# Kernel tuning notes

Measured on AMD Instinct MI355X. Metric: run time of the kernel, lower is better.

Reference implementation:

```python
import jax, jax.numpy as jnp
import numpy as np

H = 768  # bert-base hidden size; match MLP width = 2*H = 1536


def setup_inputs() -> dict:
    key = jax.random.key(0)
    ks = jax.random.split(key, 6)
    B, S = 2, 256
    std = 0.02  # TruncatedNormal(stddev=initializer_range)
    return {
        "hidden": jax.random.normal(ks[0], (B, S, H), dtype=jnp.float32),
        "w_start": jax.random.normal(ks[1], (H, 1), dtype=jnp.float32) * std,
        "b_start": jnp.zeros((1,), jnp.float32),
        "w_end": jax.random.normal(ks[2], (H, 1), dtype=jnp.float32) * std,
        "b_end": jnp.zeros((1,), jnp.float32),
        "w1": jax.random.normal(ks[3], (2 * H, 2 * H), dtype=jnp.float32) * std,
        "b1": jnp.zeros((2 * H,), jnp.float32),
        "w2": jax.random.normal(ks[4], (2 * H, 1), dtype=jnp.float32) * std,
        "b2": jnp.zeros((1,), jnp.float32),
    }


def reference(hidden, w_start, b_start, w_end, b_end, w1, b1, w2, b2):
    # hidden: [B, S, H] = BERT sequence output (dropout disabled at inference)
    start_logits = hidden @ w_start + b_start  # [B, S, 1]
    end_logits = hidden @ w_end + b_end        # [B, S, 1]

    # Pairwise span features: concat(row_i, col_j) along last dim, fed to dense1.
    # concat([row, col]) @ w1 == row @ w1[:H] + col @ w1[H:], so we split w1 and
    # broadcast-add instead of materializing the [B,S,S,2H] concat tile.
    row_proj = hidden @ w1[:H]   # [B, S, 2H] (start-token contribution)
    col_proj = hidden @ w1[H:]   # [B, S, 2H] (end-token contribution)
    pre = row_proj[:, :, None, :] + col_proj[:, None, :, :] + b1  # [B, S, S, 2H]
    act = jax.nn.gelu(pre, approximate=False)  # keras 'gelu' is exact
    match_logits = act @ w2 + b2  # [B, S, S, 1]
    return start_logits, end_logits, match_logits
```

## Files before the change

### kernel.cpp

```cpp
#include <hip/hip_runtime.h>
#include <stdint.h>

typedef __attribute__((ext_vector_type(8))) __bf16 bf16x8;
typedef __attribute__((ext_vector_type(4))) float  floatx4;
typedef __attribute__((ext_vector_type(4))) unsigned int uint4v;
typedef __attribute__((ext_vector_type(2))) unsigned int uint2v;
typedef __attribute__((ext_vector_type(4))) float  float4v;
typedef __attribute__((ext_vector_type(2))) _Float16 half2v;
typedef unsigned int u32;

__device__ __forceinline__ unsigned short f2bf(float f) {
  union { float f; unsigned int u; } x; x.f = f;
  unsigned int r = x.u + 0x7fffu + ((x.u >> 16) & 1u);
  return (unsigned short)(r >> 16);
}

__device__ __forceinline__ void gll16(const unsigned short* g, unsigned short* l) {
  __builtin_amdgcn_global_load_lds(
      (const __attribute__((address_space(1))) unsigned int*)g,
      (__attribute__((address_space(3))) unsigned int*)l, 16, 0, 0);
}

__global__ __launch_bounds__(256) void convert_kernel(
    const float* __restrict__ w1, unsigned short* __restrict__ Wfmt) {
  const int n  = blockIdx.x * 256 + threadIdx.x;
  const int qg = blockIdx.y;
  const float* src = w1 + (size_t)(qg * 8) * 1536 + n;
  uint4v o;
#pragma unroll
  for (int a = 0; a < 4; ++a) {
    u32 lo = f2bf(src[(size_t)(2 * a) * 1536]);
    u32 hi = f2bf(src[(size_t)(2 * a + 1) * 1536]);
    o[a] = lo | (hi << 16);
  }
  *(uint4v*)(Wfmt + ((size_t)qg * 1536 + n) * 8) = o;
}

__global__ __launch_bounds__(256) void proj_kernel(
    const float* __restrict__ hidden, const unsigned short* __restrict__ Wfmt,
    const float* __restrict__ b1, unsigned short* __restrict__ wsR,
    unsigned short* __restrict__ wsC,
    const float* __restrict__ w_start, const float* __restrict__ b_start,
    const float* __restrict__ w_end, const float* __restrict__ b_end,
    const float* __restrict__ b2, float* __restrict__ out) {
  const int tid  = threadIdx.x;
  if (blockIdx.y == 16) {
    if (blockIdx.x >= 32) {
      float v = b2[0];
      float4v vv = {v, v, v, v};
      int base = (blockIdx.x - 32) * 8192 + tid * 4;
#pragma unroll
      for (int itr = 0; itr < 8; ++itr)
        *(float4v*)(out + 1024 + base + itr * 1024) = vv;
      return;
    }
    const int lane = tid & 63;
    const int wv   = tid >> 6;
    const int wg   = blockIdx.x * 4 + wv;
    float wsv[12], wev[12];
#pragma unroll
    for (int t = 0; t < 12; ++t) {
      wsv[t] = w_start[lane + 64 * t];
      wev[t] = w_end[lane + 64 * t];
    }
    const float bs = b_start[0];
    const float be = b_end[0];
#pragma unroll
    for (int r = 0; r < 4; ++r) {
      int row = wg * 4 + r;
      const float* h = hidden + (size_t)row * 768;
      float ps = 0.f, pe = 0.f;
#pragma unroll
      for (int t = 0; t < 12; ++t) {
        float hv = h[lane + 64 * t];
        ps += hv * wsv[t];
        pe += hv * wev[t];
      }
#pragma unroll
      for (int off = 32; off >= 1; off >>= 1) {
        ps += __shfl_xor(ps, off, 64);
        pe += __shfl_xor(pe, off, 64);
      }
      if (lane == 0) { out[row] = ps + bs; out[512 + row] = pe + be; }
    }
    return;
  }

  __shared__ unsigned short As2[2][8 * 32 * 8];
  __shared__ unsigned short Bs2[2][8 * 64 * 8];

  const int lane = tid & 63;
  const int wave = tid >> 6;
  const int wr = wave >> 1, wc = wave & 1;
  const int m0 = blockIdx.y * 32;
  const int n0g = blockIdx.x * 64;
  const bool isR = (n0g < 1536);
  const int qgb = isR ? 0 : 96;
  const int n0 = isR ? n0g : (n0g - 1536);
  const int q4 = lane >> 4, l15 = lane & 15;

  floatx4 acc0 = {}, acc1 = {};

  const int a_row = tid >> 3;
  const int a_s   = tid & 7;
  const int aqh   = a_s >> 1;
  const int aj    = (a_s & 1) * 4;
  const float* hrow = hidden + (size_t)(m0 + a_row) * 768 + a_s * 4;

  const unsigned short* gB0 = Wfmt + ((size_t)(qgb + 2 * wave) * 1536 + n0 + lane) * 8;
  const unsigned short* gB1 = Wfmt + ((size_t)(qgb + 2 * wave + 1) * 1536 + n0 + lane) * 8;
  const size_t bstep = (size_t)8 * 1536 * 8;
  unsigned short* lB0 = &Bs2[0][(2 * wave) * 512];
  unsigned short* lB1 = &Bs2[0][(2 * wave + 1) * 512];
  unsigned short* lB0b = &Bs2[1][(2 * wave) * 512];
  unsigned short* lB1b = &Bs2[1][(2 * wave + 1) * 512];

#define PACKA(BUF, H, V)                                                     \
  {                                                                          \
    uint2v au_;                                                              \
    au_[0] = (u32)f2bf((V)[0]) | ((u32)f2bf((V)[1]) << 16);                  \
    au_[1] = (u32)f2bf((V)[2]) | ((u32)f2bf((V)[3]) << 16);                  \
    *(uint2v*)(&As2[BUF][(((H) * 4 + aqh) * 32 + a_row) * 8 + aj]) = au_;    \
  }

#define COMPUTE(BUF)                                                         \
  {                                                                          \
    _Pragma("unroll")                                                        \
    for (int ko2 = 0; ko2 < 2; ++ko2) {                                      \
      int qf = ko2 * 4 + q4;                                                 \
      bf16x8 af  = *(const bf16x8*)(&As2[BUF][(qf * 32 + 16 * wr + l15) * 8]); \
      bf16x8 bg0 = *(const bf16x8*)(&Bs2[BUF][(qf * 64 + 32 * wc + l15) * 8]); \
      bf16x8 bg1 = *(const bf16x8*)(&Bs2[BUF][(qf * 64 + 32 * wc + 16 + l15) * 8]); \
      acc0 = __builtin_amdgcn_mfma_f32_16x16x32_bf16(af, bg0, acc0, 0, 0, 0); \
      acc1 = __builtin_amdgcn_mfma_f32_16x16x32_bf16(af, bg1, acc1, 0, 0, 0); \
    }                                                                        \
  }

  gll16(gB0, lB0);
  gll16(gB1, lB1);
  float4v sA0 = *(const float4v*)(hrow);
  float4v sA1 = *(const float4v*)(hrow + 32);
  PACKA(0, 0, sA0); PACKA(0, 1, sA1);
  float4v sB0 = *(const float4v*)(hrow + 64);
  float4v sB1 = *(const float4v*)(hrow + 96);
  __syncthreads();

#pragma unroll
  for (int kb = 0; kb < 12; kb += 2) {
    if (kb + 1 < 12) {
      gll16(gB0 + (size_t)(kb + 1) * bstep, lB0b);
      gll16(gB1 + (size_t)(kb + 1) * bstep, lB1b);
      PACKA(1, 0, sB0); PACKA(1, 1, sB1);
    }
    if (kb + 2 < 12) {
      sA0 = *(const float4v*)(hrow + (kb + 2) * 64);
      sA1 = *(const float4v*)(hrow + (kb + 2) * 64 + 32);
    }
    COMPUTE(0);
    __syncthreads();
    if (kb + 2 < 12) {
      gll16(gB0 + (size_t)(kb + 2) * bstep, lB0);
      gll16(gB1 + (size_t)(kb + 2) * bstep, lB1);
      PACKA(0, 0, sA0); PACKA(0, 1, sA1);
    }
    if (kb + 3 < 12) {
      sB0 = *(const float4v*)(hrow + (kb + 3) * 64);
      sB1 = *(const float4v*)(hrow + (kb + 3) * 64 + 32);
    }
    if (kb + 1 < 12) COMPUTE(1);
    __syncthreads();
  }
#undef PACKA
#undef COMPUTE

  unsigned short* outp = isR ? wsR : wsC;
#pragma unroll
  for (int ni = 0; ni < 2; ++ni) {
    const floatx4& ac = ni ? acc1 : acc0;
    int col = n0 + 32 * wc + 16 * ni + l15;
    float bias = isR ? b1[col] : 0.0f;
#pragma unroll
    for (int r = 0; r < 4; ++r) {
      int rowg = m0 + 16 * wr + q4 * 4 + r;
      outp[(size_t)rowg * 1536 + col] = f2bf(ac[r] + bias);
    }
  }
}

__device__ __forceinline__ u32 ph_add(u32 a, u32 b) {
  u32 d; asm("v_pk_add_f16 %0, %1, %2" : "=v"(d) : "v"(a), "v"(b)); return d;
}
__device__ __forceinline__ u32 ph_mul(u32 a, u32 b) {
  u32 d; asm("v_pk_mul_f16 %0, %1, %2" : "=v"(d) : "v"(a), "v"(b)); return d;
}
__device__ __forceinline__ u32 ph_fma(u32 a, u32 b, u32 c) {
  u32 d; asm("v_pk_fma_f16 %0, %1, %2, %3" : "=v"(d) : "v"(a), "v"(b), "v"(c)); return d;
}
__device__ __forceinline__ u32 ph_max(u32 a, u32 b) {
  u32 d; asm("v_pk_max_f16 %0, %1, %2" : "=v"(d) : "v"(a), "v"(b)); return d;
}
__device__ __forceinline__ u32 ph_min(u32 a, u32 b) {
  u32 d; asm("v_pk_min_f16 %0, %1, %2" : "=v"(d) : "v"(a), "v"(b)); return d;
}
__device__ __forceinline__ u32 h2c(float f) {
  _Float16 h = (_Float16)f;
  unsigned short s = __builtin_bit_cast(unsigned short, h);
  return (u32)s | ((u32)s << 16);
}

__device__ __forceinline__ void gelu_pair(float& acc, u32 r, u32 c, u32 w,
                                          u32 C0c, u32 C1c, u32 C2c, u32 C3c,
                                          u32 LOc, u32 HIc, u32 Hc) {
  u32 x  = ph_add(r, c);
  u32 xc = ph_min(ph_max(x, LOc), HIc);
  u32 u  = ph_mul(xc, xc);
  u32 p  = ph_fma(u, ph_fma(u, ph_fma(u, C3c, C2c), C1c), C0c);
  u32 t  = ph_fma(xc, p, Hc);
  u32 g  = ph_mul(x, t);
  acc = __builtin_amdgcn_fdot2(__builtin_bit_cast(half2v, g),
                               __builtin_bit_cast(half2v, w), acc, false);
}

__device__ __forceinline__ uint4v bf8_to_h8(uint4v v) {
  uint4v o;
#pragma unroll
  for (int a = 0; a < 4; ++a) {
    union { unsigned int u; float f; } lo, hi;
    lo.u = v[a] << 16;
    hi.u = v[a] & 0xffff0000u;
    auto h = __builtin_amdgcn_cvt_pkrtz(lo.f, hi.f);
    o[a] = __builtin_bit_cast(unsigned int, h);
  }
  return o;
}

__global__ __launch_bounds__(512) void match_kernel(
    const unsigned short* __restrict__ wsR,
    const unsigned short* __restrict__ wsC,
    const float* __restrict__ w2,
    float* __restrict__ outm) {
  __shared__ u32 RsU[2][32 * 68];
  __shared__ u32 CsU[2][64 * 68];
  __shared__ u32 WsU[2][64];

  const int tid = threadIdx.x;
  const int jt = blockIdx.x;
  const int it = blockIdx.y;
  const int bz = blockIdx.z >> 2;
  const int kb4 = blockIdx.z & 3;
  const int Kb0 = kb4 * 384;

  const int rg  = tid >> 5;
  const int cg  = tid & 31;
  const int srow = tid >> 4;
  const int sseg = tid & 15;

  const u32 C0c = h2c(0.39103831f);
  const u32 C1c = h2c(-0.05415410f);
  const u32 C2c = h2c(0.00461682f);
  const u32 C3c = h2c(-1.51033e-4f);
  const u32 LOc = h2c(-3.5f);
  const u32 HIc = h2c(3.5f);
  const u32 Hc  = h2c(0.5f);

  float a0 = 0.f, a1 = 0.f, b0 = 0.f, b1 = 0.f;

  const unsigned short* gR  = wsR + (size_t)(bz * 256 + it * 32 + srow) * 1536 + sseg * 8;
  const unsigned short* gC0 = wsC + (size_t)(bz * 256 + jt * 64 + srow) * 1536 + sseg * 8;
  const unsigned short* gC1 = gC0 + (size_t)32 * 1536;

  auto wr = [&](int buf, uint4v pR, uint4v pC0, uint4v pC1, float w0, float w1) {
    *(uint4v*)(&RsU[buf][srow * 68 + sseg * 4]) = bf8_to_h8(pR);
    *(uint4v*)(&CsU[buf][srow * 68 + sseg * 4]) = bf8_to_h8(pC0);
    *(uint4v*)(&CsU[buf][(srow + 32) * 68 + sseg * 4]) = bf8_to_h8(pC1);
    if (tid < 64) {
      auto h = __builtin_amdgcn_cvt_pkrtz(w0, w1);
      WsU[buf][tid] = __builtin_bit_cast(u32, h);
    }
  };
  auto comp = [&](int buf) {
    const u32* rap = &RsU[buf][(2 * rg) * 68];
    const u32* rbp = rap + 68;
    const u32* c0p = &CsU[buf][cg * 68];
    const u32* c1p = c0p + 32 * 68;
    const u32* wp  = &WsU[buf][0];
#pragma unroll 4
    for (int ks = 0; ks < 16; ++ks) {
      uint4v ra = *(const uint4v*)(rap + ks * 4);
      uint4v rb = *(const uint4v*)(rbp + ks * 4);
      uint4v wv = *(const uint4v*)(wp + ks * 4);
      uint4v cv = *(const uint4v*)(c0p + ks * 4);
#pragma unroll
      for (int p = 0; p < 4; ++p) {
        gelu_pair(a0, ra[p], cv[p], wv[p], C0c, C1c, C2c, C3c, LOc, HIc, Hc);
        gelu_pair(b0, rb[p], cv[p], wv[p], C0c, C1c, C2c, C3c, LOc, HIc, Hc);
      }
      uint4v cw = *(const uint4v*)(c1p + ks * 4);
#pragma unroll
      for (int p = 0; p < 4; ++p) {
        gelu_pair(a1, ra[p], cw[p], wv[p], C0c, C1c, C2c, C3c, LOc, HIc, Hc);
        gelu_pair(b1, rb[p], cw[p], wv[p], C0c, C1c, C2c, C3c, LOc, HIc, Hc);
      }
    }
  };

  uint4v pR  = *(const uint4v*)(gR + Kb0);
  uint4v pC0 = *(const uint4v*)(gC0 + Kb0);
  uint4v pC1 = *(const uint4v*)(gC1 + Kb0);
  float pw0 = 0.f, pw1 = 0.f;
  if (tid < 64) { pw0 = w2[Kb0 + 2 * tid]; pw1 = w2[Kb0 + 2 * tid + 1]; }
  wr(0, pR, pC0, pC1, pw0, pw1);
  __syncthreads();

  pR  = *(const uint4v*)(gR + Kb0 + 128);
  pC0 = *(const uint4v*)(gC0 + Kb0 + 128);
  pC1 = *(const uint4v*)(gC1 + Kb0 + 128);
  if (tid < 64) { pw0 = w2[Kb0 + 128 + 2 * tid]; pw1 = w2[Kb0 + 128 + 2 * tid + 1]; }
  comp(0);
  wr(1, pR, pC0, pC1, pw0, pw1);
  __syncthreads();

  pR  = *(const uint4v*)(gR + Kb0 + 256);
  pC0 = *(const uint4v*)(gC0 + Kb0 + 256);
  pC1 = *(const uint4v*)(gC1 + Kb0 + 256);
  if (tid < 64) { pw0 = w2[Kb0 + 256 + 2 * tid]; pw1 = w2[Kb0 + 256 + 2 * tid + 1]; }
  comp(1);
  wr(0, pR, pC0, pC1, pw0, pw1);
  __syncthreads();

  comp(0);

  const size_t rowA = (size_t)(bz * 256 + it * 32 + 2 * rg);
  const size_t base = rowA * 256 + jt * 64 + cg;
  unsafeAtomicAdd(&outm[base +  0], a0);
  unsafeAtomicAdd(&outm[base + 32], a1);
  unsafeAtomicAdd(&outm[base + 256 +  0], b0);
  unsafeAtomicAdd(&outm[base + 256 + 32], b1);
}

extern "C" void kernel_launch(void* const* d_in, const int* in_sizes, int n_in,
                              void* d_out, int out_size, void* d_ws, size_t ws_size,
                              hipStream_t stream) {
  const float* hidden  = (const float*)d_in[0];
  const float* w_start = (const float*)d_in[1];
  const float* b_start = (const float*)d_in[2];
  const float* w_end   = (const float*)d_in[3];
  const float* b_end   = (const float*)d_in[4];
  const float* w1      = (const float*)d_in[5];
  const float* b1      = (const float*)d_in[6];
  const float* w2      = (const float*)d_in[7];
  const float* b2      = (const float*)d_in[8];

  float* out = (float*)d_out;
  char* ws = (char*)d_ws;
  unsigned short* wsR  = (unsigned short*)(ws);
  unsigned short* wsC  = (unsigned short*)(ws + 1572864);
  unsigned short* Wfmt = (unsigned short*)(ws + 3145728);

  convert_kernel<<<dim3(6, 192), dim3(256), 0, stream>>>(w1, Wfmt);
  proj_kernel<<<dim3(48, 17), dim3(256), 0, stream>>>(
      hidden, Wfmt, b1, wsR, wsC, w_start, b_start, w_end, b_end, b2, out);
  match_kernel<<<dim3(4, 8, 8), dim3(512), 0, stream>>>(wsR, wsC, w2, out + 1024);
}
```

Baseline: 123.6 us.

## Store projections as fp16 and split match kernel K into 12 bands

The projection kernel now writes its intermediate row/col projections as fp16 instead of bf16, so the match kernel copies them straight into shared memory without a per-element bf16-to-fp16 conversion. The match kernel's K split goes from 4 bands of 384 to 12 bands of 128. That triples the grid and shrinks the shared-memory tiles, raising occupancy and parallelism. In exchange it triples the atomic adds into the output, and fp16 has less range than bf16 for the projections.

```diff
diff --git a/kernel.cpp b/kernel.cpp
--- a/kernel.cpp
+++ b/kernel.cpp
@@ -182,7 +182,8 @@
 #pragma unroll
     for (int r = 0; r < 4; ++r) {
       int rowg = m0 + 16 * wr + q4 * 4 + r;
-      outp[(size_t)rowg * 1536 + col] = f2bf(ac[r] + bias);
+      _Float16 h = (_Float16)(ac[r] + bias);
+      outp[(size_t)rowg * 1536 + col] = __builtin_bit_cast(unsigned short, h);
     }
   }
 }
@@ -221,39 +222,26 @@
                                __builtin_bit_cast(half2v, w), acc, false);
 }
 
-__device__ __forceinline__ uint4v bf8_to_h8(uint4v v) {
-  uint4v o;
-#pragma unroll
-  for (int a = 0; a < 4; ++a) {
-    union { unsigned int u; float f; } lo, hi;
-    lo.u = v[a] << 16;
-    hi.u = v[a] & 0xffff0000u;
-    auto h = __builtin_amdgcn_cvt_pkrtz(lo.f, hi.f);
-    o[a] = __builtin_bit_cast(unsigned int, h);
-  }
-  return o;
-}
-
 __global__ __launch_bounds__(512) void match_kernel(
     const unsigned short* __restrict__ wsR,
     const unsigned short* __restrict__ wsC,
     const float* __restrict__ w2,
     float* __restrict__ outm) {
-  __shared__ u32 RsU[2][32 * 68];
-  __shared__ u32 CsU[2][64 * 68];
-  __shared__ u32 WsU[2][64];
+  __shared__ u32 RsU[2][32 * 36];
+  __shared__ u32 CsU[2][64 * 36];
+  __shared__ u32 WsU[2][32];
 
   const int tid = threadIdx.x;
   const int jt = blockIdx.x;
   const int it = blockIdx.y;
-  const int bz = blockIdx.z >> 2;
-  const int kb4 = blockIdx.z & 3;
-  const int Kb0 = kb4 * 384;
+  const int bz = blockIdx.z / 12;
+  const int band = blockIdx.z % 12;
+  const int Kb0 = band * 128;
 
   const int rg  = tid >> 5;
   const int cg  = tid & 31;
-  const int srow = tid >> 4;
-  const int sseg = tid & 15;
+  const int srow = tid >> 3;
+  const int sseg = tid & 7;
 
   const u32 C0c = h2c(0.39103831f);
   const u32 C1c = h2c(-0.05415410f);
@@ -265,27 +253,28 @@
 
   float a0 = 0.f, a1 = 0.f, b0 = 0.f, b1 = 0.f;
 
-  const unsigned short* gR  = wsR + (size_t)(bz * 256 + it * 32 + srow) * 1536 + sseg * 8;
-  const unsigned short* gC0 = wsC + (size_t)(bz * 256 + jt * 64 + srow) * 1536 + sseg * 8;
-  const unsigned short* gC1 = gC0 + (size_t)32 * 1536;
-
-  auto wr = [&](int buf, uint4v pR, uint4v pC0, uint4v pC1, float w0, float w1) {
-    *(uint4v*)(&RsU[buf][srow * 68 + sseg * 4]) = bf8_to_h8(pR);
-    *(uint4v*)(&CsU[buf][srow * 68 + sseg * 4]) = bf8_to_h8(pC0);
-    *(uint4v*)(&CsU[buf][(srow + 32) * 68 + sseg * 4]) = bf8_to_h8(pC1);
-    if (tid < 64) {
-      auto h = __builtin_amdgcn_cvt_pkrtz(w0, w1);
+  const bool doR = (tid < 256);
+  const unsigned short* gR =
+      wsR + (size_t)(bz * 256 + it * 32 + (srow & 31)) * 1536 + Kb0 + sseg * 8;
+  const unsigned short* gC =
+      wsC + (size_t)(bz * 256 + jt * 64 + srow) * 1536 + Kb0 + sseg * 8;
+
+  auto wrbuf = [&](int buf, uint4v pR, uint4v pC, float w0, float w1v) {
+    if (doR) *(uint4v*)(&RsU[buf][(srow & 31) * 36 + sseg * 4]) = pR;
+    *(uint4v*)(&CsU[buf][srow * 36 + sseg * 4]) = pC;
+    if (tid < 32) {
+      auto h = __builtin_amdgcn_cvt_pkrtz(w0, w1v);
       WsU[buf][tid] = __builtin_bit_cast(u32, h);
     }
   };
   auto comp = [&](int buf) {
-    const u32* rap = &RsU[buf][(2 * rg) * 68];
-    const u32* rbp = rap + 68;
-    const u32* c0p = &CsU[buf][cg * 68];
-    const u32* c1p = c0p + 32 * 68;
+    const u32* rap = &RsU[buf][(2 * rg) * 36];
+    const u32* rbp = rap + 36;
+    const u32* c0p = &CsU[buf][cg * 36];
+    const u32* c1p = c0p + 32 * 36;
     const u32* wp  = &WsU[buf][0];
-#pragma unroll 4
-    for (int ks = 0; ks < 16; ++ks) {
+#pragma unroll
+    for (int ks = 0; ks < 8; ++ks) {
       uint4v ra = *(const uint4v*)(rap + ks * 4);
       uint4v rb = *(const uint4v*)(rbp + ks * 4);
       uint4v wv = *(const uint4v*)(wp + ks * 4);
@@ -304,31 +293,22 @@
     }
   };
 
-  uint4v pR  = *(const uint4v*)(gR + Kb0);
-  uint4v pC0 = *(const uint4v*)(gC0 + Kb0);
-  uint4v pC1 = *(const uint4v*)(gC1 + Kb0);
+  uint4v pR = {}, pC;
   float pw0 = 0.f, pw1 = 0.f;
-  if (tid < 64) { pw0 = w2[Kb0 + 2 * tid]; pw1 = w2[Kb0 + 2 * tid + 1]; }
-  wr(0, pR, pC0, pC1, pw0, pw1);
+  if (doR) pR = *(const uint4v*)(gR);
+  pC = *(const uint4v*)(gC);
+  if (tid < 32) { pw0 = w2[Kb0 + 2 * tid]; pw1 = w2[Kb0 + 2 * tid + 1]; }
+  wrbuf(0, pR, pC, pw0, pw1);
   __syncthreads();
 
-  pR  = *(const uint4v*)(gR + Kb0 + 128);
-  pC0 = *(const uint4v*)(gC0 + Kb0 + 128);
-  pC1 = *(const uint4v*)(gC1 + Kb0 + 128);
-  if (tid < 64) { pw0 = w2[Kb0 + 128 + 2 * tid]; pw1 = w2[Kb0 + 128 + 2 * tid + 1]; }
+  if (doR) pR = *(const uint4v*)(gR + 64);
+  pC = *(const uint4v*)(gC + 64);
+  if (tid < 32) { pw0 = w2[Kb0 + 64 + 2 * tid]; pw1 = w2[Kb0 + 64 + 2 * tid + 1]; }
   comp(0);
-  wr(1, pR, pC0, pC1, pw0, pw1);
+  wrbuf(1, pR, pC, pw0, pw1);
   __syncthreads();
 
-  pR  = *(const uint4v*)(gR + Kb0 + 256);
-  pC0 = *(const uint4v*)(gC0 + Kb0 + 256);
-  pC1 = *(const uint4v*)(gC1 + Kb0 + 256);
-  if (tid < 64) { pw0 = w2[Kb0 + 256 + 2 * tid]; pw1 = w2[Kb0 + 256 + 2 * tid + 1]; }
   comp(1);
-  wr(0, pR, pC0, pC1, pw0, pw1);
-  __syncthreads();
-
-  comp(0);
 
   const size_t rowA = (size_t)(bz * 256 + it * 32 + 2 * rg);
   const size_t base = rowA * 256 + jt * 64 + cg;
@@ -360,5 +340,5 @@
   convert_kernel<<<dim3(6, 192), dim3(256), 0, stream>>>(w1, Wfmt);
   proj_kernel<<<dim3(48, 17), dim3(256), 0, stream>>>(
       hidden, Wfmt, b1, wsR, wsC, w_start, b_start, w_end, b_end, b2, out);
-  match_kernel<<<dim3(4, 8, 8), dim3(512), 0, stream>>>(wsR, wsC, w2, out + 1024);
-}
+  match_kernel<<<dim3(4, 8, 24), dim3(512), 0, stream>>>(wsR, wsC, w2, out + 1024);
+}
```

After: 126.0 us. About the same (+2.0%).
